# Performance work log

Measured on AMD Instinct MI355X. Metric: run time of the kernel, lower is better.

## Reference

```python
import jax, jax.numpy as jnp
import numpy as np

PENETRATION_W = 10.0
STABILITY_W = 1.0
ENERGY_W = 0.1
MIN_DIST = 0.05

B, T, N, D = 16, 100, 128, 3

def setup_inputs() -> dict:
    key = jax.random.key(0)
    k1, k2, k3 = jax.random.split(key, 3)
    trajectories = jax.random.normal(k1, (B, T, N, D), dtype=jnp.float32)
    velocities = jax.random.normal(k2, (B, T, N, D), dtype=jnp.float32)
    forces = jax.random.normal(k3, (B, T, N, D), dtype=jnp.float32)
    return {"trajectories": trajectories, "velocities": velocities, "forces": forces}

def _penetration_loss(trajectories):
    b, t, n, _ = trajectories.shape
    pos = trajectories[..., :3]                                   # [B,T,N,3]
    diff = pos[:, :, :, None, :] - pos[:, :, None, :, :]          # [B,T,N,N,3]
    d2 = jnp.sum(diff * diff, axis=-1)                            # [B,T,N,N]
    mask = jnp.triu(jnp.ones((n, n), dtype=bool), k=1)            # strictly i<j
    # avoid sqrt(0) on diagonal for safe gradients; masked out below
    dist = jnp.sqrt(jnp.where(mask, d2, 1.0))
    pen = jax.nn.relu(MIN_DIST - dist) * mask                     # [B,T,N,N]
    # original: sum over (t, i<j) of mean over batch
    total = jnp.mean(jnp.sum(pen, axis=(1, 2, 3)))
    return total / (t * n * (n - 1) / 2)

def _stability_loss(velocities):
    return jnp.mean(jnp.linalg.norm(velocities[:, -5:], axis=-1))

def _energy_loss(positions, velocities, forces):
    kinetic_start = 0.5 * jnp.mean(jnp.sum(velocities[:, 0] ** 2, axis=-1))
    kinetic_end = 0.5 * jnp.mean(jnp.sum(velocities[:, -1] ** 2, axis=-1))
    displacements = positions[:, 1:] - positions[:, :-1]
    work = jnp.mean(jnp.sum(forces[:, :-1] * displacements, axis=-1))
    return jnp.abs(kinetic_end - kinetic_start - work)

def reference(trajectories, velocities, forces):
    loss = PENETRATION_W * _penetration_loss(trajectories)
    loss = loss + STABILITY_W * _stability_loss(velocities)
    loss = loss + ENERGY_W * _energy_loss(trajectories, velocities, forces)
    return loss
```

## Files before the change

### kernel.cpp

```cpp
#include <hip/hip_runtime.h>
#include <math.h>

constexpr int B = 16, T = 100, N = 128;
constexpr float MIN_DIST  = 0.05f;
constexpr float MIN_DIST2 = MIN_DIST * MIN_DIST;

constexpr int THREADS      = 256;
constexpr int PEN_BLOCKS   = B * T;
constexpr int MISC_BLOCKS  = 160;
constexpr int TOTAL_BLOCKS = PEN_BLOCKS + MISC_BLOCKS;

constexpr int PER_B = T * N * 3;
constexpr int PER_T = N * 3;

constexpr int WORK_V4_PER_B = (T - 1) * N * 3 / 4;
constexpr int WORK_V4 = B * WORK_V4_PER_B;
constexpr int KE_V4_PER_SLICE = N * 3 / 4;
constexpr int KE_V4  = 2 * B * KE_V4_PER_SLICE;
constexpr int STAB_V = B * 5 * N;
constexpr int MISC_TOTAL = WORK_V4 + STAB_V + KE_V4;

constexpr int WORK_N = B * (T - 1) * N;

constexpr int WORK_OFF = 1600, STAB_OFF = 1760, KE0_OFF = 1920, KE1_OFF = 2080;

__device__ __forceinline__ float wave_sum(float v) {
#pragma unroll
    for (int off = 32; off > 0; off >>= 1) v += __shfl_down(v, off, 64);
    return v;
}

__global__ __launch_bounds__(THREADS) void physics_fused(
    const float* __restrict__ traj, const float* __restrict__ vel,
    const float* __restrict__ frc, float* __restrict__ ws)
{
    __shared__ float4 spos[N];
    __shared__ float  red[4][4];

    const int tid  = threadIdx.x;
    const int bid  = blockIdx.x;
    const int lane = tid & 63;
    const int wv   = tid >> 6;

    if (bid < PEN_BLOCKS) {
        const float* p = traj + (size_t)bid * PER_T;
        for (int k = tid; k < N; k += THREADS)
            spos[k] = make_float4(p[k * 3], p[k * 3 + 1], p[k * 3 + 2], 0.f);
        __syncthreads();

        const float4 pa = spos[lane];
        const float4 pb = spos[lane + 64];
        const int jbase = wv * 32;
        float s = 0.f;
#pragma unroll 8
        for (int jj = 0; jj < 32; ++jj) {
            const int j = jbase + jj;
            const float4 pj = spos[j];
            const float dxa = pa.x - pj.x, dya = pa.y - pj.y, dza = pa.z - pj.z;
            const float d2a = dxa * dxa + dya * dya + dza * dza;
            const float dxb = pb.x - pj.x, dyb = pb.y - pj.y, dzb = pb.z - pj.z;
            const float d2b = dxb * dxb + dyb * dyb + dzb * dzb;
            const bool ha = (d2a < MIN_DIST2) & (j != lane);
            const bool hb = (d2b < MIN_DIST2) & (j != lane + 64);
            if (__builtin_expect(__any(ha | hb), 0)) {
                if (ha) s += MIN_DIST - sqrtf(d2a);
                if (hb) s += MIN_DIST - sqrtf(d2b);
            }
        }
        float w = wave_sum(s);
        if (lane == 0) red[0][wv] = w;
        __syncthreads();
        if (tid == 0)
            ws[bid] = 0.5f * (red[0][0] + red[0][1] + red[0][2] + red[0][3]);
    } else {
        const int mb = bid - PEN_BLOCKS;
        const float4* t4 = (const float4*)traj;
        const float4* f4 = (const float4*)frc;
        const float4* v4 = (const float4*)vel;
        float sw = 0.f, ss = 0.f, k0 = 0.f, k1 = 0.f;
        const int stride = MISC_BLOCKS * THREADS;
        for (int v = mb * THREADS + tid; v < MISC_TOTAL; v += stride) {
            if (v < WORK_V4) {
                const int b = v / WORK_V4_PER_B;
                const int r = v - b * WORK_V4_PER_B;
                const int base = b * (PER_B / 4) + r;
                const float4 f  = f4[base];
                const float4 t0 = t4[base];
                const float4 t1 = t4[base + PER_T / 4];
                sw += f.x * (t1.x - t0.x) + f.y * (t1.y - t0.y)
                    + f.z * (t1.z - t0.z) + f.w * (t1.w - t0.w);
            } else if (v < WORK_V4 + STAB_V) {
                const int s2 = v - WORK_V4;
                const int b  = s2 / 640;
                const int r  = s2 - b * 640;
                const int e  = b * PER_B + 95 * PER_T + r * 3;
                const float vx = vel[e], vy = vel[e + 1], vz = vel[e + 2];
                ss += sqrtf(vx * vx + vy * vy + vz * vz);
            } else {
                const int s2    = v - WORK_V4 - STAB_V;
                const int which = s2 / 1536;
                const int rr    = s2 - which * 1536;
                const int b     = rr / KE_V4_PER_SLICE;
                const int r     = rr - b * KE_V4_PER_SLICE;
                const float4 q  = v4[b * (PER_B / 4) + which * (99 * PER_T / 4) + r];
                const float k   = q.x * q.x + q.y * q.y + q.z * q.z + q.w * q.w;
                if (which) k1 += k; else k0 += k;
            }
        }
        float vals[4] = {sw, ss, k0, k1};
#pragma unroll
        for (int vv = 0; vv < 4; ++vv) {
            float w = wave_sum(vals[vv]);
            if (lane == 0) red[vv][wv] = w;
        }
        __syncthreads();
        if (tid == 0) {
            ws[WORK_OFF + mb] = red[0][0] + red[0][1] + red[0][2] + red[0][3];
            ws[STAB_OFF + mb] = red[1][0] + red[1][1] + red[1][2] + red[1][3];
            ws[KE0_OFF  + mb] = red[2][0] + red[2][1] + red[2][2] + red[2][3];
            ws[KE1_OFF  + mb] = red[3][0] + red[3][1] + red[3][2] + red[3][3];
        }
    }
}

__global__ __launch_bounds__(256) void physics_finalize(
    const float* __restrict__ ws, float* __restrict__ out)
{
    __shared__ float redP[4], redM[4];
    const int tid = threadIdx.x, lane = tid & 63, wv = tid >> 6;

    float p = 0.f;
    for (int i = tid; i < PEN_BLOCKS; i += 256) p += ws[i];

    const int base = WORK_OFF + 160 * wv;
    float m = ws[base + lane] + ws[base + 64 + lane]
            + (lane < 32 ? ws[base + 128 + lane] : 0.f);

    p = wave_sum(p);
    m = wave_sum(m);
    if (lane == 0) { redP[wv] = p; redM[wv] = m; }
    __syncthreads();

    if (tid == 0) {
        const float pen = redP[0] + redP[1] + redP[2] + redP[3];
        const float wk = redM[0], st = redM[1], k0 = redM[2], k1 = redM[3];
        const float pen_loss  = pen / (float)((long long)B * T * (N * (N - 1) / 2));
        const float stab_loss = st / (float)STAB_V;
        const float ke_s = 0.5f * k0 / (float)(B * N);
        const float ke_e = 0.5f * k1 / (float)(B * N);
        const float work = wk / (float)WORK_N;
        out[0] = 10.0f * pen_loss + stab_loss + 0.1f * fabsf(ke_e - ke_s - work);
    }
}

extern "C" void kernel_launch(void* const* d_in, const int* in_sizes, int n_in,
                              void* d_out, int out_size, void* d_ws, size_t ws_size,
                              hipStream_t stream) {
    const float* traj = (const float*)d_in[0];
    const float* vel  = (const float*)d_in[1];
    const float* frc  = (const float*)d_in[2];
    float* out = (float*)d_out;
    float* ws  = (float*)d_ws;

    physics_fused<<<TOTAL_BLOCKS, THREADS, 0, stream>>>(traj, vel, frc, ws);
    physics_finalize<<<1, 256, 0, stream>>>(ws, out);
}
```

Baseline: 69.81 us.

## Merge both kernels into one cooperative launch with grid sync and pair-symmetric penetration

```diff
diff --git a/kernel.cpp b/kernel.cpp
--- a/kernel.cpp
+++ b/kernel.cpp
@@ -1,14 +1,15 @@
 #include <hip/hip_runtime.h>
+#include <hip/hip_cooperative_groups.h>
 #include <math.h>
+
+namespace cg = cooperative_groups;
 
 constexpr int B = 16, T = 100, N = 128;
 constexpr float MIN_DIST  = 0.05f;
 constexpr float MIN_DIST2 = MIN_DIST * MIN_DIST;
 
-constexpr int THREADS      = 256;
-constexpr int PEN_BLOCKS   = B * T;
-constexpr int MISC_BLOCKS  = 160;
-constexpr int TOTAL_BLOCKS = PEN_BLOCKS + MISC_BLOCKS;
+constexpr int THREADS = 256;
+constexpr int GRID    = 800;
 
 constexpr int PER_B = T * N * 3;
 constexpr int PER_T = N * 3;
@@ -22,7 +23,7 @@
 
 constexpr int WORK_N = B * (T - 1) * N;
 
-constexpr int WORK_OFF = 1600, STAB_OFF = 1760, KE0_OFF = 1920, KE1_OFF = 2080;
+constexpr int SEG_PEN = 0, SEG_WORK = 1, SEG_STAB = 2, SEG_KE0 = 3, SEG_KE1 = 4;
 
 __device__ __forceinline__ float wave_sum(float v) {
 #pragma unroll
@@ -30,126 +31,139 @@
     return v;
 }
 
-__global__ __launch_bounds__(THREADS) void physics_fused(
+__global__ __launch_bounds__(THREADS, 4) void physics_one(
     const float* __restrict__ traj, const float* __restrict__ vel,
-    const float* __restrict__ frc, float* __restrict__ ws)
+    const float* __restrict__ frc, float* __restrict__ ws, float* __restrict__ out)
 {
-    __shared__ float4 spos[N];
-    __shared__ float  red[4][4];
+    __shared__ float  sraw[2 * PER_T];
+    __shared__ float4 spos[2 * N];
+    __shared__ float  red[5][4];
 
     const int tid  = threadIdx.x;
     const int bid  = blockIdx.x;
     const int lane = tid & 63;
     const int wv   = tid >> 6;
 
-    if (bid < PEN_BLOCKS) {
-        const float* p = traj + (size_t)bid * PER_T;
-        for (int k = tid; k < N; k += THREADS)
-            spos[k] = make_float4(p[k * 3], p[k * 3 + 1], p[k * 3 + 2], 0.f);
-        __syncthreads();
+    float4 stg = make_float4(0.f, 0.f, 0.f, 0.f);
+    if (tid < 192) stg = ((const float4*)traj)[bid * 192 + tid];
 
-        const float4 pa = spos[lane];
-        const float4 pb = spos[lane + 64];
-        const int jbase = wv * 32;
-        float s = 0.f;
+    float sw = 0.f, ss = 0.f, kk0 = 0.f, kk1 = 0.f;
+    {
+        const int v = bid * THREADS + tid;
+        if (v < WORK_V4) {
+            const int b = v / WORK_V4_PER_B;
+            const int r = v - b * WORK_V4_PER_B;
+            const int base = b * (PER_B / 4) + r;
+            const float4 f  = ((const float4*)frc)[base];
+            const float4 t0 = ((const float4*)traj)[base];
+            const float4 t1 = ((const float4*)traj)[base + PER_T / 4];
+            sw = f.x * (t1.x - t0.x) + f.y * (t1.y - t0.y)
+               + f.z * (t1.z - t0.z) + f.w * (t1.w - t0.w);
+        } else if (v < WORK_V4 + STAB_V) {
+            const int s2 = v - WORK_V4;
+            const int b  = s2 / 640;
+            const int r  = s2 - b * 640;
+            const int e  = b * PER_B + 95 * PER_T + r * 3;
+            const float vx = vel[e], vy = vel[e + 1], vz = vel[e + 2];
+            ss = sqrtf(vx * vx + vy * vy + vz * vz);
+        } else if (v < MISC_TOTAL) {
+            const int s2    = v - WORK_V4 - STAB_V;
+            const int which = s2 / 1536;
+            const int rr    = s2 - which * 1536;
+            const int b     = rr / KE_V4_PER_SLICE;
+            const int r     = rr - b * KE_V4_PER_SLICE;
+            const float4 q  = ((const float4*)vel)[b * (PER_B / 4) + which * (99 * PER_T / 4) + r];
+            const float k   = q.x * q.x + q.y * q.y + q.z * q.z + q.w * q.w;
+            if (which) kk1 = k; else kk0 = k;
+        }
+    }
+
+    if (tid < 192) ((float4*)sraw)[tid] = stg;
+    __syncthreads();
+    spos[tid] = make_float4(sraw[3 * tid], sraw[3 * tid + 1], sraw[3 * tid + 2], 0.f);
+    __syncthreads();
+
+    const int i    = tid & (N - 1);
+    const int half = tid >> 7;
+    const float4 p0 = spos[i];
+    const float4 p1 = spos[N + i];
+    float s = 0.f;
+    const int klo = 1 + half * 32;
+    const int khi = 32 + half * 31;
 #pragma unroll 8
-        for (int jj = 0; jj < 32; ++jj) {
-            const int j = jbase + jj;
-            const float4 pj = spos[j];
-            const float dxa = pa.x - pj.x, dya = pa.y - pj.y, dza = pa.z - pj.z;
-            const float d2a = dxa * dxa + dya * dya + dza * dza;
-            const float dxb = pb.x - pj.x, dyb = pb.y - pj.y, dzb = pb.z - pj.z;
-            const float d2b = dxb * dxb + dyb * dyb + dzb * dzb;
-            const bool ha = (d2a < MIN_DIST2) & (j != lane);
-            const bool hb = (d2b < MIN_DIST2) & (j != lane + 64);
-            if (__builtin_expect(__any(ha | hb), 0)) {
-                if (ha) s += MIN_DIST - sqrtf(d2a);
-                if (hb) s += MIN_DIST - sqrtf(d2b);
-            }
+    for (int k = klo; k <= khi; ++k) {
+        const int j = (i + k) & (N - 1);
+        const float4 q0 = spos[j];
+        const float4 q1 = spos[N + j];
+        float dx = p0.x - q0.x, dy = p0.y - q0.y, dz = p0.z - q0.z;
+        const float d2a = dx * dx + dy * dy + dz * dz;
+        dx = p1.x - q1.x; dy = p1.y - q1.y; dz = p1.z - q1.z;
+        const float d2b = dx * dx + dy * dy + dz * dz;
+        const bool ha = d2a < MIN_DIST2;
+        const bool hb = d2b < MIN_DIST2;
+        if (__builtin_expect(__any(ha | hb), 0)) {
+            if (ha) s += MIN_DIST - sqrtf(d2a);
+            if (hb) s += MIN_DIST - sqrtf(d2b);
         }
-        float w = wave_sum(s);
-        if (lane == 0) red[0][wv] = w;
-        __syncthreads();
-        if (tid == 0)
-            ws[bid] = 0.5f * (red[0][0] + red[0][1] + red[0][2] + red[0][3]);
-    } else {
-        const int mb = bid - PEN_BLOCKS;
-        const float4* t4 = (const float4*)traj;
-        const float4* f4 = (const float4*)frc;
-        const float4* v4 = (const float4*)vel;
-        float sw = 0.f, ss = 0.f, k0 = 0.f, k1 = 0.f;
-        const int stride = MISC_BLOCKS * THREADS;
-        for (int v = mb * THREADS + tid; v < MISC_TOTAL; v += stride) {
-            if (v < WORK_V4) {
-                const int b = v / WORK_V4_PER_B;
-                const int r = v - b * WORK_V4_PER_B;
-                const int base = b * (PER_B / 4) + r;
-                const float4 f  = f4[base];
-                const float4 t0 = t4[base];
-                const float4 t1 = t4[base + PER_T / 4];
-                sw += f.x * (t1.x - t0.x) + f.y * (t1.y - t0.y)
-                    + f.z * (t1.z - t0.z) + f.w * (t1.w - t0.w);
-            } else if (v < WORK_V4 + STAB_V) {
-                const int s2 = v - WORK_V4;
-                const int b  = s2 / 640;
-                const int r  = s2 - b * 640;
-                const int e  = b * PER_B + 95 * PER_T + r * 3;
-                const float vx = vel[e], vy = vel[e + 1], vz = vel[e + 2];
-                ss += sqrtf(vx * vx + vy * vy + vz * vz);
-            } else {
-                const int s2    = v - WORK_V4 - STAB_V;
-                const int which = s2 / 1536;
-                const int rr    = s2 - which * 1536;
-                const int b     = rr / KE_V4_PER_SLICE;
-                const int r     = rr - b * KE_V4_PER_SLICE;
-                const float4 q  = v4[b * (PER_B / 4) + which * (99 * PER_T / 4) + r];
-                const float k   = q.x * q.x + q.y * q.y + q.z * q.z + q.w * q.w;
-                if (which) k1 += k; else k0 += k;
-            }
+    }
+    if (half) {
+        const int j = (i + 64) & (N - 1);
+        const float4 q0 = spos[j];
+        const float4 q1 = spos[N + j];
+        float dx = p0.x - q0.x, dy = p0.y - q0.y, dz = p0.z - q0.z;
+        const float d2a = dx * dx + dy * dy + dz * dz;
+        dx = p1.x - q1.x; dy = p1.y - q1.y; dz = p1.z - q1.z;
+        const float d2b = dx * dx + dy * dy + dz * dz;
+        const bool ha = (d2a < MIN_DIST2) & (i < 64);
+        const bool hb = (d2b < MIN_DIST2) & (i < 64);
+        if (__builtin_expect(__any(ha | hb), 0)) {
+            if (ha) s += MIN_DIST - sqrtf(d2a);
+            if (hb) s += MIN_DIST - sqrtf(d2b);
         }
-        float vals[4] = {sw, ss, k0, k1};
+    }
+
+    float vals[5] = {s, sw, ss, kk0, kk1};
 #pragma unroll
-        for (int vv = 0; vv < 4; ++vv) {
-            float w = wave_sum(vals[vv]);
-            if (lane == 0) red[vv][wv] = w;
+    for (int vv = 0; vv < 5; ++vv) {
+        const float w = wave_sum(vals[vv]);
+        if (lane == 0) red[vv][wv] = w;
+    }
+    __syncthreads();
+    if (tid == 0) {
+#pragma unroll
+        for (int vv = 0; vv < 5; ++vv)
+            ws[vv * GRID + bid] = red[vv][0] + red[vv][1] + red[vv][2] + red[vv][3];
+    }
+    __threadfence();
+
+    cg::this_grid().sync();
+
+    if (bid == 0) {
+        float acc[5];
+#pragma unroll
+        for (int seg = 0; seg < 5; ++seg) {
+            float a = 0.f;
+            for (int idx = tid; idx < GRID; idx += THREADS) a += ws[seg * GRID + idx];
+            acc[seg] = wave_sum(a);
+        }
+        if (lane == 0) {
+#pragma unroll
+            for (int seg = 0; seg < 5; ++seg) red[seg][wv] = acc[seg];
         }
         __syncthreads();
         if (tid == 0) {
-            ws[WORK_OFF + mb] = red[0][0] + red[0][1] + red[0][2] + red[0][3];
-            ws[STAB_OFF + mb] = red[1][0] + red[1][1] + red[1][2] + red[1][3];
-            ws[KE0_OFF  + mb] = red[2][0] + red[2][1] + red[2][2] + red[2][3];
-            ws[KE1_OFF  + mb] = red[3][0] + red[3][1] + red[3][2] + red[3][3];
+            const float pen = red[0][0] + red[0][1] + red[0][2] + red[0][3];
+            const float wk  = red[1][0] + red[1][1] + red[1][2] + red[1][3];
+            const float st  = red[2][0] + red[2][1] + red[2][2] + red[2][3];
+            const float k0  = red[3][0] + red[3][1] + red[3][2] + red[3][3];
+            const float k1  = red[4][0] + red[4][1] + red[4][2] + red[4][3];
+            const float pen_loss  = pen / (float)((long long)B * T * (N * (N - 1) / 2));
+            const float stab_loss = st / (float)STAB_V;
+            const float ke_s = 0.5f * k0 / (float)(B * N);
+            const float ke_e = 0.5f * k1 / (float)(B * N);
+            const float work = wk / (float)WORK_N;
+            out[0] = 10.0f * pen_loss + stab_loss + 0.1f * fabsf(ke_e - ke_s - work);
         }
-    }
-}
-
-__global__ __launch_bounds__(256) void physics_finalize(
-    const float* __restrict__ ws, float* __restrict__ out)
-{
-    __shared__ float redP[4], redM[4];
-    const int tid = threadIdx.x, lane = tid & 63, wv = tid >> 6;
-
-    float p = 0.f;
-    for (int i = tid; i < PEN_BLOCKS; i += 256) p += ws[i];
-
-    const int base = WORK_OFF + 160 * wv;
-    float m = ws[base + lane] + ws[base + 64 + lane]
-            + (lane < 32 ? ws[base + 128 + lane] : 0.f);
-
-    p = wave_sum(p);
-    m = wave_sum(m);
-    if (lane == 0) { redP[wv] = p; redM[wv] = m; }
-    __syncthreads();
-
-    if (tid == 0) {
-        const float pen = redP[0] + redP[1] + redP[2] + redP[3];
-        const float wk = redM[0], st = redM[1], k0 = redM[2], k1 = redM[3];
-        const float pen_loss  = pen / (float)((long long)B * T * (N * (N - 1) / 2));
-        const float stab_loss = st / (float)STAB_V;
-        const float ke_s = 0.5f * k0 / (float)(B * N);
-        const float ke_e = 0.5f * k1 / (float)(B * N);
-        const float work = wk / (float)WORK_N;
-        out[0] = 10.0f * pen_loss + stab_loss + 0.1f * fabsf(ke_e - ke_s - work);
     }
 }
 
@@ -162,6 +176,7 @@
     float* out = (float*)d_out;
     float* ws  = (float*)d_ws;
 
-    physics_fused<<<TOTAL_BLOCKS, THREADS, 0, stream>>>(traj, vel, frc, ws);
-    physics_finalize<<<1, 256, 0, stream>>>(ws, out);
+    void* args[] = {(void*)&traj, (void*)&vel, (void*)&frc, (void*)&ws, (void*)&out};
+    hipLaunchCooperativeKernel((const void*)physics_one, dim3(GRID), dim3(THREADS),
+                               args, 0, stream);
 }
```

Measured after the change: 168.6 us. +141.5%, slower.
